# Performance work log

Measured on AMD Instinct MI355X. Metric: run time of the kernel, lower is better.

Reference implementation:

```python
import jax, jax.numpy as jnp
import numpy as np

PI = np.pi
WIN = (8, 8)
N = WIN[0] * WIN[1]          # 64 tokens per window
NUM_HEADS = 8
DIM = 256
HEAD_DIM = DIM // NUM_HEADS  # 32
P = 4                        # Fourier series order (hardcoded in module)
W_RES = 64                   # input_resolution[1]
SCALE = HEAD_DIM ** -0.5
B_ = 1024                    # num_windows * batch


def _azimuth():
    # relative_coords[:, :, 1] from the torch module: relative column offsets
    ch = np.arange(WIN[0])
    cw = np.arange(WIN[1])
    gh, gw = np.meshgrid(ch, cw, indexing='ij')
    cf = np.stack([gh.ravel(), gw.ravel()])          # (2, N)
    rel = cf[:, :, None] - cf[:, None, :]            # (2, N, N)
    return jnp.asarray(rel[1], dtype=jnp.float32)    # (N, N)


def setup_inputs() -> dict:
    key = jax.random.key(0)
    ks = jax.random.split(key, 12)
    std = 0.02
    return {
        'x': jax.random.normal(ks[0], (B_, N, DIM), dtype=jnp.float32),
        'D': jax.random.uniform(ks[1], (B_, N), dtype=jnp.float32),
        'a_p': std * jax.random.normal(ks[2], (P + 1, NUM_HEADS), dtype=jnp.float32),
        'b_p': std * jax.random.normal(ks[3], (P, NUM_HEADS), dtype=jnp.float32),
        'a_r': std * jax.random.normal(ks[4], (P + 1, NUM_HEADS), dtype=jnp.float32),
        'b_r': std * jax.random.normal(ks[5], (P, NUM_HEADS), dtype=jnp.float32),
        'qkv_w': std * jax.random.normal(ks[6], (3 * DIM, DIM), dtype=jnp.float32),
        'qkv_b': jnp.zeros((3 * DIM,), dtype=jnp.float32),
        'proj_w': std * jax.random.normal(ks[7], (DIM, DIM), dtype=jnp.float32),
        'proj_b': jnp.zeros((DIM,), dtype=jnp.float32),
    }


def reference(x, D, a_p, b_p, a_r, b_r, qkv_w, qkv_b, proj_w, proj_b):
    B, n, C = x.shape

    # ---- azimuth Fourier bias: A_phi, shape (H, N, N) ----
    az = _azimuth() * (2.0 * PI / W_RES)                       # (N, N)
    ii = jnp.arange(1, P + 1, dtype=x.dtype)[:, None, None]    # (P, 1, 1)
    cosP = jnp.cos(ii * az)                                    # (P, N, N)
    sinP = jnp.sin(ii * az)
    A_phi = (jnp.einsum('ph,pij->hij', a_p[1:], cosP)
             + jnp.einsum('ph,pij->hij', b_p, sinP)) / P + a_p[0][:, None, None]

    # ---- radius Fourier bias: A_r, shape (B, N, N, H); rad[b,i,j] = D[b,j] - D[b,i] ----
    rad = D[:, None, :] - D[:, :, None]                        # (B, N, N)
    r_max = 2.0                                                # module overwrites r_max = 2
    A_r = jnp.zeros(rad.shape + (NUM_HEADS,), dtype=x.dtype)
    for i in range(1, P + 1):
        arg = rad * (2.0 * PI * i / r_max)
        A_r = A_r + jnp.cos(arg)[..., None] * a_r[i] + jnp.sin(arg)[..., None] * b_r[i - 1]
    A_r = A_r / P + a_r[0]                                     # (B, N, N, H)

    # ---- attention ----
    qkv = (x @ qkv_w.T + qkv_b).reshape(B, n, 3, NUM_HEADS, HEAD_DIM)
    qkv = qkv.transpose(2, 0, 3, 1, 4)                         # (3, B, H, N, hd)
    q, k, v = qkv[0], qkv[1], qkv[2]
    attn = jnp.einsum('bhid,bhjd->bhij', q * SCALE, k)
    attn = attn + A_phi[None] + A_r.transpose(0, 3, 1, 2)
    attn = jax.nn.softmax(attn, axis=-1)
    out = jnp.einsum('bhij,bhjd->bhid', attn, v)
    out = out.transpose(0, 2, 1, 3).reshape(B, n, C)
    return out @ proj_w.T + proj_b
```

## Files before the change

### kernel.cpp

```cpp
#include <hip/hip_runtime.h>
#include <hip/hip_bf16.h>


using short8  = __attribute__((ext_vector_type(8))) short;
using floatx4 = __attribute__((ext_vector_type(4))) float;

#define PI_F    3.14159265358979323846f
#define SCALE_F 0.17677669529663687f

__global__ void prep_kernel(const float* __restrict__ qw,
                            const float* __restrict__ pw,
                            __hip_bfloat16* __restrict__ dst) {
  int g = blockIdx.x * 256 + threadIdx.x;
  const float4* src;
  __hip_bfloat16* d;
  if (g < 49152) { src = (const float4*)qw + g; d = dst + g * 4; }
  else { int g2 = g - 49152; src = (const float4*)pw + g2; d = dst + 196608 + g2 * 4; }
  float4 v = *src;
  d[0] = __float2bfloat16(v.x);
  d[1] = __float2bfloat16(v.y);
  d[2] = __float2bfloat16(v.z);
  d[3] = __float2bfloat16(v.w);
}

__device__ __forceinline__ void fourier_feats(float dv, int col, float* f) {
  float s1, c1; __sincosf(PI_F * dv, &s1, &c1);
  float c2 = c1*c1 - s1*s1, s2 = 2.f*s1*c1;
  float c3 = c2*c1 - s2*s1, s3 = s2*c1 + c2*s1;
  float c4 = c2*c2 - s2*s2, s4 = 2.f*s2*c2;
  float sa1, ca1; __sincosf((2.f * PI_F / 64.f) * (float)col, &sa1, &ca1);
  float ca2 = ca1*ca1 - sa1*sa1, sa2 = 2.f*sa1*ca1;
  float ca3 = ca2*ca1 - sa2*sa1, sa3 = sa2*ca1 + ca2*sa1;
  float ca4 = ca2*ca2 - sa2*sa2, sa4 = 2.f*sa2*ca2;
  f[0]=c1;  f[1]=c2;  f[2]=c3;  f[3]=c4;
  f[4]=s1;  f[5]=s2;  f[6]=s3;  f[7]=s4;
  f[8]=ca1; f[9]=ca2; f[10]=ca3; f[11]=ca4;
  f[12]=sa1; f[13]=sa2; f[14]=sa3; f[15]=sa4;
}

__global__ __launch_bounds__(512, 2) void fused_kernel(
    const float* __restrict__ x, const float* __restrict__ D,
    const float* __restrict__ a_p, const float* __restrict__ b_p,
    const float* __restrict__ a_r, const float* __restrict__ b_r,
    const __hip_bfloat16* __restrict__ wq, const float* __restrict__ qkv_b,
    const __hip_bfloat16* __restrict__ pwb, const float* __restrict__ pb,
    float* __restrict__ out)
{
  constexpr int LDX = 264, LDQ = 264, LDK = 264, LDQf = 40, LDKm = 136,
                LDVt = 72, LDP = 72, LDO = 264;
  __shared__ __align__(16) __hip_bfloat16 sScr[64 * 264];
  __shared__ __align__(16) __hip_bfloat16 sQ  [64 * 264];
  __shared__ __align__(16) __hip_bfloat16 sK  [64 * 264];
  __shared__ __align__(16) __hip_bfloat16 sQf [64 * 40];
  __shared__ __align__(16) __hip_bfloat16 sKm [64 * 136];
  __shared__ __align__(16) __hip_bfloat16 sVt [256 * 72];

  const int tid = threadIdx.x;
  const int lane = tid & 63, w = tid >> 6;
  const int laneN = lane & 15, laneQ = lane >> 4;
  const int b = blockIdx.x;
  const floatx4 fzero = {0.f, 0.f, 0.f, 0.f};
  const short8 zero8 = {0, 0, 0, 0, 0, 0, 0, 0};

  const float4* xg = (const float4*)(x + (size_t)b * 16384);
  #pragma unroll
  for (int it = 0; it < 8; ++it) {
    int g = tid + it * 512;
    float4 v = xg[g];
    int t = g >> 6, c = (g & 63) * 4;
    __hip_bfloat16* p = &sScr[t * LDX + c];
    p[0] = __float2bfloat16(v.x); p[1] = __float2bfloat16(v.y);
    p[2] = __float2bfloat16(v.z); p[3] = __float2bfloat16(v.w);
  }
  if (tid < 64) {
    float f[16];
    fourier_feats(D[b * 64 + tid], tid & 7, f);
    #pragma unroll
    for (int i = 0; i < 16; ++i) sQf[tid * LDQf + i] = __float2bfloat16(f[i]);
    #pragma unroll
    for (int i = 16; i < 32; ++i) sQf[tid * LDQf + i] = __float2bfloat16(0.f);
  }
  __syncthreads();

  {
    int t = tid >> 3, hh = tid & 7;
    float f[16];
    fourier_feats(D[b * 64 + t], t & 7, f);
    #pragma unroll
    for (int p = 0; p < 4; ++p) {
      float ar = a_r[(p + 1) * 8 + hh], br = b_r[p * 8 + hh];
      float ap = a_p[(p + 1) * 8 + hh], bp = b_p[p * 8 + hh];
      float cr = f[p], sr = f[4 + p], ca = f[8 + p], sa = f[12 + p];
      sKm[t * LDKm + hh * 16 +  0 + p] = __float2bfloat16((ar * cr + br * sr) * 0.25f);
      sKm[t * LDKm + hh * 16 +  4 + p] = __float2bfloat16((ar * sr - br * cr) * 0.25f);
      sKm[t * LDKm + hh * 16 +  8 + p] = __float2bfloat16((ap * ca - bp * sa) * 0.25f);
      sKm[t * LDKm + hh * 16 + 12 + p] = __float2bfloat16((ap * sa + bp * ca) * 0.25f);
    }
  }

  short8 afq[4][8];
  #pragma unroll
  for (int mt = 0; mt < 4; ++mt)
    #pragma unroll
    for (int kk = 0; kk < 8; ++kk)
      afq[mt][kk] = *(const short8*)&sScr[(mt * 16 + laneN) * LDX + kk * 32 + laneQ * 8];

  #pragma unroll
  for (int ni = 0; ni < 6; ++ni) {
    int col0 = (w * 6 + ni) * 16;
    float bias = qkv_b[col0 + laneN];
    short8 bq[8];
    #pragma unroll
    for (int kk = 0; kk < 8; ++kk)
      bq[kk] = *(const short8*)&wq[(size_t)(col0 + laneN) * 256 + kk * 32 + laneQ * 8];
    floatx4 acc[4] = {fzero, fzero, fzero, fzero};
    #pragma unroll
    for (int kk = 0; kk < 8; ++kk)
      #pragma unroll
      for (int mt = 0; mt < 4; ++mt)
        acc[mt] = __builtin_amdgcn_mfma_f32_16x16x32_bf16(afq[mt][kk], bq[kk], acc[mt], 0, 0, 0);
    if (col0 < 256) {
      #pragma unroll
      for (int mt = 0; mt < 4; ++mt)
        #pragma unroll
        for (int r = 0; r < 4; ++r)
          sQ[(mt * 16 + laneQ * 4 + r) * LDQ + col0 + laneN] =
              __float2bfloat16((acc[mt][r] + bias) * SCALE_F);
    } else if (col0 < 512) {
      #pragma unroll
      for (int mt = 0; mt < 4; ++mt)
        #pragma unroll
        for (int r = 0; r < 4; ++r)
          sK[(mt * 16 + laneQ * 4 + r) * LDK + (col0 - 256) + laneN] =
              __float2bfloat16(acc[mt][r] + bias);
    } else {
      int vd = col0 - 512 + laneN;
      #pragma unroll
      for (int mt = 0; mt < 4; ++mt)
        #pragma unroll
        for (int r = 0; r < 4; ++r)
          sVt[vd * LDVt + (mt * 16 + laneQ * 4 + r)] = __float2bfloat16(acc[mt][r] + bias);
    }
  }
  __syncthreads();

  const int h = w;
  short8 qf0[4], qf1[4], kf0[4], kf1[4];
  #pragma unroll
  for (int mt = 0; mt < 4; ++mt) {
    qf0[mt] = *(const short8*)&sQ[(mt * 16 + laneN) * LDQ + h * 32 + laneQ * 8];
    qf1[mt] = *(const short8*)&sQf[(mt * 16 + laneN) * LDQf + laneQ * 8];
  }
  #pragma unroll
  for (int nt = 0; nt < 4; ++nt) {
    kf0[nt] = *(const short8*)&sK[(nt * 16 + laneN) * LDK + h * 32 + laneQ * 8];
    short8 km = *(const short8*)&sKm[(nt * 16 + laneN) * LDKm + h * 16 + (laneQ & 1) * 8];
    kf1[nt] = (laneQ < 2) ? km : zero8;
  }
  floatx4 s[4][4];
  #pragma unroll
  for (int mt = 0; mt < 4; ++mt)
    #pragma unroll
    for (int nt = 0; nt < 4; ++nt) {
      s[mt][nt] = __builtin_amdgcn_mfma_f32_16x16x32_bf16(qf0[mt], kf0[nt], fzero, 0, 0, 0);
      s[mt][nt] = __builtin_amdgcn_mfma_f32_16x16x32_bf16(qf1[mt], kf1[nt], s[mt][nt], 0, 0, 0);
    }

  short8 vb[2][2];
  #pragma unroll
  for (int ont = 0; ont < 2; ++ont)
    #pragma unroll
    for (int kk = 0; kk < 2; ++kk)
      vb[ont][kk] = *(const short8*)&sVt[(h * 32 + ont * 16 + laneN) * LDVt + kk * 32 + laneQ * 8];

  floatx4 oacc[4][2];
  __hip_bfloat16* Pw = &sScr[w * 16 * LDP];
  #pragma unroll
  for (int mt = 0; mt < 4; ++mt) {
    #pragma unroll
    for (int r = 0; r < 4; ++r) {
      float mx = fmaxf(fmaxf(s[mt][0][r], s[mt][1][r]), fmaxf(s[mt][2][r], s[mt][3][r]));
      mx = fmaxf(mx, __shfl_xor(mx, 1));
      mx = fmaxf(mx, __shfl_xor(mx, 2));
      mx = fmaxf(mx, __shfl_xor(mx, 4));
      mx = fmaxf(mx, __shfl_xor(mx, 8));
      float e0 = __expf(s[mt][0][r] - mx), e1 = __expf(s[mt][1][r] - mx);
      float e2 = __expf(s[mt][2][r] - mx), e3 = __expf(s[mt][3][r] - mx);
      float sum = e0 + e1 + e2 + e3;
      sum += __shfl_xor(sum, 1);
      sum += __shfl_xor(sum, 2);
      sum += __shfl_xor(sum, 4);
      sum += __shfl_xor(sum, 8);
      float inv = __builtin_amdgcn_rcpf(sum);
      int pr = laneQ * 4 + r;
      Pw[pr * LDP +  0 + laneN] = __float2bfloat16(e0 * inv);
      Pw[pr * LDP + 16 + laneN] = __float2bfloat16(e1 * inv);
      Pw[pr * LDP + 32 + laneN] = __float2bfloat16(e2 * inv);
      Pw[pr * LDP + 48 + laneN] = __float2bfloat16(e3 * inv);
    }
    short8 pf0 = *(const short8*)&Pw[laneN * LDP + laneQ * 8];
    short8 pf1 = *(const short8*)&Pw[laneN * LDP + 32 + laneQ * 8];
    #pragma unroll
    for (int ont = 0; ont < 2; ++ont) {
      oacc[mt][ont] = __builtin_amdgcn_mfma_f32_16x16x32_bf16(pf0, vb[ont][0], fzero, 0, 0, 0);
      oacc[mt][ont] = __builtin_amdgcn_mfma_f32_16x16x32_bf16(pf1, vb[ont][1], oacc[mt][ont], 0, 0, 0);
    }
  }
  __syncthreads();

  #pragma unroll
  for (int mt = 0; mt < 4; ++mt)
    #pragma unroll
    for (int ont = 0; ont < 2; ++ont)
      #pragma unroll
      for (int r = 0; r < 4; ++r)
        sScr[(mt * 16 + laneQ * 4 + r) * LDO + h * 32 + ont * 16 + laneN] =
            __float2bfloat16(oacc[mt][ont][r]);
  __syncthreads();

  const int col0 = w * 32;
  floatx4 pacc[4][2];
  #pragma unroll
  for (int mt = 0; mt < 4; ++mt) { pacc[mt][0] = fzero; pacc[mt][1] = fzero; }
  #pragma unroll
  for (int kk = 0; kk < 8; ++kk) {
    short8 pa[4], pbf[2];
    #pragma unroll
    for (int mt = 0; mt < 4; ++mt)
      pa[mt] = *(const short8*)&sScr[(mt * 16 + laneN) * LDO + kk * 32 + laneQ * 8];
    #pragma unroll
    for (int n2 = 0; n2 < 2; ++n2)
      pbf[n2] = *(const short8*)&pwb[(size_t)(col0 + n2 * 16 + laneN) * 256 + kk * 32 + laneQ * 8];
    #pragma unroll
    for (int mt = 0; mt < 4; ++mt)
      #pragma unroll
      for (int n2 = 0; n2 < 2; ++n2)
        pacc[mt][n2] = __builtin_amdgcn_mfma_f32_16x16x32_bf16(pa[mt], pbf[n2], pacc[mt][n2], 0, 0, 0);
  }
  float bias0 = pb[col0 + laneN], bias1 = pb[col0 + 16 + laneN];
  float* og = out + (size_t)b * 16384;
  #pragma unroll
  for (int mt = 0; mt < 4; ++mt)
    #pragma unroll
    for (int n2 = 0; n2 < 2; ++n2)
      #pragma unroll
      for (int r = 0; r < 4; ++r)
        og[(mt * 16 + laneQ * 4 + r) * 256 + col0 + n2 * 16 + laneN] =
            pacc[mt][n2][r] + (n2 ? bias1 : bias0);
}

extern "C" void kernel_launch(void* const* d_in, const int* in_sizes, int n_in,
                              void* d_out, int out_size, void* d_ws, size_t ws_size,
                              hipStream_t stream) {
  const float* x      = (const float*)d_in[0];
  const float* D      = (const float*)d_in[1];
  const float* a_p    = (const float*)d_in[2];
  const float* b_p    = (const float*)d_in[3];
  const float* a_r    = (const float*)d_in[4];
  const float* b_r    = (const float*)d_in[5];
  const float* qkv_w  = (const float*)d_in[6];
  const float* qkv_b  = (const float*)d_in[7];
  const float* proj_w = (const float*)d_in[8];
  const float* proj_b = (const float*)d_in[9];

  __hip_bfloat16* wq  = (__hip_bfloat16*)d_ws;
  __hip_bfloat16* pwb = wq + 196608;
  float* out = (float*)d_out;

  prep_kernel<<<256, 256, 0, stream>>>(qkv_w, proj_w, wq);
  fused_kernel<<<1024, 512, 0, stream>>>(x, D, a_p, b_p, a_r, b_r, wq, qkv_b,
                                         pwb, proj_b, out);
}
```

Measured before the change: 210.8 us.

## Restructure fused attention to 4 waves, two heads per wave, per-head QKV

Halves the block to 256 threads. Each wave now computes QKV projection columns for its own two heads directly from global x, so the block-wide shared staging of x and the barrier between projection and attention go away. Fourier bias fragments are computed in registers rather than through shared memory, and LDS is shrunk to per-wave Q/K/Vt/P scratch that is reused as the output buffer. The prep kernel packs 8 bf16 per store. In exchange, x is re-read from global/L2 by every wave for each head (eight times per block instead of once), and register pressure rises from the 6x4 accumulators.

```diff
diff --git a/kernel.cpp b/kernel.cpp
--- a/kernel.cpp
+++ b/kernel.cpp
@@ -7,38 +7,30 @@
 
 #define PI_F    3.14159265358979323846f
 #define SCALE_F 0.17677669529663687f
+
+__device__ __forceinline__ short bsh(float x) {
+  __hip_bfloat16 h = __float2bfloat16(x);
+  return *reinterpret_cast<short*>(&h);
+}
+__device__ __forceinline__ short8 pack8(float4 a, float4 b) {
+  short8 r;
+  r[0] = bsh(a.x); r[1] = bsh(a.y); r[2] = bsh(a.z); r[3] = bsh(a.w);
+  r[4] = bsh(b.x); r[5] = bsh(b.y); r[6] = bsh(b.z); r[7] = bsh(b.w);
+  return r;
+}
 
 __global__ void prep_kernel(const float* __restrict__ qw,
                             const float* __restrict__ pw,
                             __hip_bfloat16* __restrict__ dst) {
   int g = blockIdx.x * 256 + threadIdx.x;
   const float4* src;
-  __hip_bfloat16* d;
-  if (g < 49152) { src = (const float4*)qw + g; d = dst + g * 4; }
-  else { int g2 = g - 49152; src = (const float4*)pw + g2; d = dst + 196608 + g2 * 4; }
-  float4 v = *src;
-  d[0] = __float2bfloat16(v.x);
-  d[1] = __float2bfloat16(v.y);
-  d[2] = __float2bfloat16(v.z);
-  d[3] = __float2bfloat16(v.w);
-}
-
-__device__ __forceinline__ void fourier_feats(float dv, int col, float* f) {
-  float s1, c1; __sincosf(PI_F * dv, &s1, &c1);
-  float c2 = c1*c1 - s1*s1, s2 = 2.f*s1*c1;
-  float c3 = c2*c1 - s2*s1, s3 = s2*c1 + c2*s1;
-  float c4 = c2*c2 - s2*s2, s4 = 2.f*s2*c2;
-  float sa1, ca1; __sincosf((2.f * PI_F / 64.f) * (float)col, &sa1, &ca1);
-  float ca2 = ca1*ca1 - sa1*sa1, sa2 = 2.f*sa1*ca1;
-  float ca3 = ca2*ca1 - sa2*sa1, sa3 = sa2*ca1 + ca2*sa1;
-  float ca4 = ca2*ca2 - sa2*sa2, sa4 = 2.f*sa2*ca2;
-  f[0]=c1;  f[1]=c2;  f[2]=c3;  f[3]=c4;
-  f[4]=s1;  f[5]=s2;  f[6]=s3;  f[7]=s4;
-  f[8]=ca1; f[9]=ca2; f[10]=ca3; f[11]=ca4;
-  f[12]=sa1; f[13]=sa2; f[14]=sa3; f[15]=sa4;
-}
-
-__global__ __launch_bounds__(512, 2) void fused_kernel(
+  short8* d;
+  if (g < 24576) { src = (const float4*)qw + 2 * g; d = (short8*)dst + g; }
+  else { int g2 = g - 24576; src = (const float4*)pw + 2 * g2; d = (short8*)(dst + 196608) + g2; }
+  *d = pack8(src[0], src[1]);
+}
+
+__global__ __launch_bounds__(256, 2) void fused_kernel(
     const float* __restrict__ x, const float* __restrict__ D,
     const float* __restrict__ a_p, const float* __restrict__ b_p,
     const float* __restrict__ a_r, const float* __restrict__ b_r,
@@ -46,14 +38,7 @@
     const __hip_bfloat16* __restrict__ pwb, const float* __restrict__ pb,
     float* __restrict__ out)
 {
-  constexpr int LDX = 264, LDQ = 264, LDK = 264, LDQf = 40, LDKm = 136,
-                LDVt = 72, LDP = 72, LDO = 264;
-  __shared__ __align__(16) __hip_bfloat16 sScr[64 * 264];
-  __shared__ __align__(16) __hip_bfloat16 sQ  [64 * 264];
-  __shared__ __align__(16) __hip_bfloat16 sK  [64 * 264];
-  __shared__ __align__(16) __hip_bfloat16 sQf [64 * 40];
-  __shared__ __align__(16) __hip_bfloat16 sKm [64 * 136];
-  __shared__ __align__(16) __hip_bfloat16 sVt [256 * 72];
+  __shared__ __align__(16) __hip_bfloat16 sLds[4 * 7424];
 
   const int tid = threadIdx.x;
   const int lane = tid & 63, w = tid >> 6;
@@ -62,191 +47,222 @@
   const floatx4 fzero = {0.f, 0.f, 0.f, 0.f};
   const short8 zero8 = {0, 0, 0, 0, 0, 0, 0, 0};
 
-  const float4* xg = (const float4*)(x + (size_t)b * 16384);
-  #pragma unroll
-  for (int it = 0; it < 8; ++it) {
-    int g = tid + it * 512;
-    float4 v = xg[g];
-    int t = g >> 6, c = (g & 63) * 4;
-    __hip_bfloat16* p = &sScr[t * LDX + c];
-    p[0] = __float2bfloat16(v.x); p[1] = __float2bfloat16(v.y);
-    p[2] = __float2bfloat16(v.z); p[3] = __float2bfloat16(v.w);
-  }
-  if (tid < 64) {
-    float f[16];
-    fourier_feats(D[b * 64 + tid], tid & 7, f);
-    #pragma unroll
-    for (int i = 0; i < 16; ++i) sQf[tid * LDQf + i] = __float2bfloat16(f[i]);
-    #pragma unroll
-    for (int i = 16; i < 32; ++i) sQf[tid * LDQf + i] = __float2bfloat16(0.f);
-  }
+  __hip_bfloat16* Q  = &sLds[w * 7424];
+  __hip_bfloat16* K  = Q + 2560;
+  __hip_bfloat16* Vt = Q + 5120;
+  __hip_bfloat16* Pp = Q;
+  __hip_bfloat16* sO = &sLds[0];
+
+  const float* xb = x + (size_t)b * 16384;
+
+  float f8[4][8];
+  short8 qf1[4];
+  {
+    float sa1, ca1; __sincosf((2.f * PI_F / 64.f) * (float)(laneN & 7), &sa1, &ca1);
+    float ca2 = ca1*ca1 - sa1*sa1, sa2 = 2.f*sa1*ca1;
+    float ca3 = ca2*ca1 - sa2*sa1, sa3 = sa2*ca1 + ca2*sa1;
+    float ca4 = ca2*ca2 - sa2*sa2, sa4 = 2.f*sa2*ca2;
+    short8 qaz;
+    qaz[0]=bsh(ca1); qaz[1]=bsh(ca2); qaz[2]=bsh(ca3); qaz[3]=bsh(ca4);
+    qaz[4]=bsh(sa1); qaz[5]=bsh(sa2); qaz[6]=bsh(sa3); qaz[7]=bsh(sa4);
+    #pragma unroll
+    for (int tt = 0; tt < 4; ++tt) {
+      float dv = D[b * 64 + tt * 16 + laneN];
+      float s1, c1; __sincosf(PI_F * dv, &s1, &c1);
+      float c2 = c1*c1 - s1*s1, s2 = 2.f*s1*c1;
+      float c3 = c2*c1 - s2*s1, s3 = s2*c1 + c2*s1;
+      float c4 = c2*c2 - s2*s2, s4 = 2.f*s2*c2;
+      if (laneQ == 0) {
+        f8[tt][0]=c1; f8[tt][1]=c2; f8[tt][2]=c3; f8[tt][3]=c4;
+        f8[tt][4]=s1; f8[tt][5]=s2; f8[tt][6]=s3; f8[tt][7]=s4;
+      } else {
+        f8[tt][0]=ca1; f8[tt][1]=ca2; f8[tt][2]=ca3; f8[tt][3]=ca4;
+        f8[tt][4]=sa1; f8[tt][5]=sa2; f8[tt][6]=sa3; f8[tt][7]=sa4;
+      }
+      short8 qrad;
+      qrad[0]=bsh(c1); qrad[1]=bsh(c2); qrad[2]=bsh(c3); qrad[3]=bsh(c4);
+      qrad[4]=bsh(s1); qrad[5]=bsh(s2); qrad[6]=bsh(s3); qrad[7]=bsh(s4);
+      qf1[tt] = (laneQ == 0) ? qrad : ((laneQ == 1) ? qaz : zero8);
+    }
+  }
+
+  floatx4 oacc[2][4][2];
+
+  #pragma unroll
+  for (int hi = 0; hi < 2; ++hi) {
+    const int h = w * 2 + hi;
+
+    int col0s[6];
+    #pragma unroll
+    for (int ni = 0; ni < 6; ++ni)
+      col0s[ni] = (ni < 2) ? h * 32 + ni * 16
+                : (ni < 4) ? 256 + h * 32 + (ni - 2) * 16
+                           : 512 + h * 32 + (ni - 4) * 16;
+    floatx4 acc[6][4];
+    #pragma unroll
+    for (int ni = 0; ni < 6; ++ni)
+      #pragma unroll
+      for (int mt = 0; mt < 4; ++mt) acc[ni][mt] = fzero;
+
+    #pragma unroll
+    for (int kk = 0; kk < 8; ++kk) {
+      short8 a4[4];
+      #pragma unroll
+      for (int mt = 0; mt < 4; ++mt) {
+        const float4* p = (const float4*)(xb + (mt * 16 + laneN) * 256 + kk * 32 + laneQ * 8);
+        a4[mt] = pack8(p[0], p[1]);
+      }
+      #pragma unroll
+      for (int ni = 0; ni < 6; ++ni) {
+        short8 bq = *(const short8*)&wq[(size_t)(col0s[ni] + laneN) * 256 + kk * 32 + laneQ * 8];
+        #pragma unroll
+        for (int mt = 0; mt < 4; ++mt)
+          acc[ni][mt] = __builtin_amdgcn_mfma_f32_16x16x32_bf16(a4[mt], bq, acc[ni][mt], 0, 0, 0);
+      }
+    }
+    #pragma unroll
+    for (int ni = 0; ni < 6; ++ni) {
+      float bias = qkv_b[col0s[ni] + laneN];
+      #pragma unroll
+      for (int mt = 0; mt < 4; ++mt)
+        #pragma unroll
+        for (int r = 0; r < 4; ++r) {
+          int row = mt * 16 + laneQ * 4 + r;
+          float v = acc[ni][mt][r] + bias;
+          if (ni < 2)
+            Q[row * 40 + ni * 16 + laneN] = __float2bfloat16(v * SCALE_F);
+          else if (ni < 4)
+            K[row * 40 + (ni - 2) * 16 + laneN] = __float2bfloat16(v);
+          else
+            Vt[((ni - 4) * 16 + laneN) * 72 + row] = __float2bfloat16(v);
+        }
+    }
+
+    short8 kf1[4];
+    {
+      float A[4], Bp[4];
+      #pragma unroll
+      for (int j = 0; j < 4; ++j) {
+        float arj = a_r[(j + 1) * 8 + h], apj = a_p[(j + 1) * 8 + h];
+        float brj = b_r[j * 8 + h],       bpj = b_p[j * 8 + h];
+        A[j]  = 0.25f * ((laneQ == 0) ? arj : apj);
+        Bp[j] = 0.25f * ((laneQ == 0) ? brj : -bpj);
+      }
+      #pragma unroll
+      for (int tt = 0; tt < 4; ++tt) {
+        short8 m;
+        #pragma unroll
+        for (int j = 0; j < 4; ++j) {
+          m[j]     = bsh(A[j] * f8[tt][j]     + Bp[j] * f8[tt][4 + j]);
+          m[4 + j] = bsh(A[j] * f8[tt][4 + j] - Bp[j] * f8[tt][j]);
+        }
+        kf1[tt] = (laneQ < 2) ? m : zero8;
+      }
+    }
+
+    short8 qf0[4], kf0[4], vb[2][2];
+    #pragma unroll
+    for (int mt = 0; mt < 4; ++mt)
+      qf0[mt] = *(const short8*)&Q[(mt * 16 + laneN) * 40 + laneQ * 8];
+    #pragma unroll
+    for (int nt = 0; nt < 4; ++nt)
+      kf0[nt] = *(const short8*)&K[(nt * 16 + laneN) * 40 + laneQ * 8];
+    #pragma unroll
+    for (int ont = 0; ont < 2; ++ont)
+      #pragma unroll
+      for (int kk = 0; kk < 2; ++kk)
+        vb[ont][kk] = *(const short8*)&Vt[(ont * 16 + laneN) * 72 + kk * 32 + laneQ * 8];
+
+    floatx4 s[4][4];
+    #pragma unroll
+    for (int mt = 0; mt < 4; ++mt)
+      #pragma unroll
+      for (int nt = 0; nt < 4; ++nt) {
+        s[mt][nt] = __builtin_amdgcn_mfma_f32_16x16x32_bf16(qf0[mt], kf0[nt], fzero, 0, 0, 0);
+        s[mt][nt] = __builtin_amdgcn_mfma_f32_16x16x32_bf16(qf1[mt], kf1[nt], s[mt][nt], 0, 0, 0);
+      }
+
+    #pragma unroll
+    for (int mt = 0; mt < 4; ++mt) {
+      #pragma unroll
+      for (int r = 0; r < 4; ++r) {
+        float mx = fmaxf(fmaxf(s[mt][0][r], s[mt][1][r]), fmaxf(s[mt][2][r], s[mt][3][r]));
+        mx = fmaxf(mx, __shfl_xor(mx, 1));
+        mx = fmaxf(mx, __shfl_xor(mx, 2));
+        mx = fmaxf(mx, __shfl_xor(mx, 4));
+        mx = fmaxf(mx, __shfl_xor(mx, 8));
+        float e0 = __expf(s[mt][0][r] - mx), e1 = __expf(s[mt][1][r] - mx);
+        float e2 = __expf(s[mt][2][r] - mx), e3 = __expf(s[mt][3][r] - mx);
+        float sum = e0 + e1 + e2 + e3;
+        sum += __shfl_xor(sum, 1);
+        sum += __shfl_xor(sum, 2);
+        sum += __shfl_xor(sum, 4);
+        sum += __shfl_xor(sum, 8);
+        float inv = __builtin_amdgcn_rcpf(sum);
+        int row = mt * 16 + laneQ * 4 + r;
+        Pp[row * 72 +  0 + laneN] = __float2bfloat16(e0 * inv);
+        Pp[row * 72 + 16 + laneN] = __float2bfloat16(e1 * inv);
+        Pp[row * 72 + 32 + laneN] = __float2bfloat16(e2 * inv);
+        Pp[row * 72 + 48 + laneN] = __float2bfloat16(e3 * inv);
+      }
+    }
+
+    #pragma unroll
+    for (int mt = 0; mt < 4; ++mt) {
+      short8 pf0 = *(const short8*)&Pp[(mt * 16 + laneN) * 72 + laneQ * 8];
+      short8 pf1 = *(const short8*)&Pp[(mt * 16 + laneN) * 72 + 32 + laneQ * 8];
+      #pragma unroll
+      for (int ont = 0; ont < 2; ++ont) {
+        oacc[hi][mt][ont] = __builtin_amdgcn_mfma_f32_16x16x32_bf16(pf0, vb[ont][0], fzero, 0, 0, 0);
+        oacc[hi][mt][ont] = __builtin_amdgcn_mfma_f32_16x16x32_bf16(pf1, vb[ont][1], oacc[hi][mt][ont], 0, 0, 0);
+      }
+    }
+  }
+
   __syncthreads();
-
-  {
-    int t = tid >> 3, hh = tid & 7;
-    float f[16];
-    fourier_feats(D[b * 64 + t], t & 7, f);
-    #pragma unroll
-    for (int p = 0; p < 4; ++p) {
-      float ar = a_r[(p + 1) * 8 + hh], br = b_r[p * 8 + hh];
-      float ap = a_p[(p + 1) * 8 + hh], bp = b_p[p * 8 + hh];
-      float cr = f[p], sr = f[4 + p], ca = f[8 + p], sa = f[12 + p];
-      sKm[t * LDKm + hh * 16 +  0 + p] = __float2bfloat16((ar * cr + br * sr) * 0.25f);
-      sKm[t * LDKm + hh * 16 +  4 + p] = __float2bfloat16((ar * sr - br * cr) * 0.25f);
-      sKm[t * LDKm + hh * 16 +  8 + p] = __float2bfloat16((ap * ca - bp * sa) * 0.25f);
-      sKm[t * LDKm + hh * 16 + 12 + p] = __float2bfloat16((ap * sa + bp * ca) * 0.25f);
-    }
-  }
-
-  short8 afq[4][8];
+  #pragma unroll
+  for (int hi = 0; hi < 2; ++hi)
+    #pragma unroll
+    for (int mt = 0; mt < 4; ++mt)
+      #pragma unroll
+      for (int ont = 0; ont < 2; ++ont)
+        #pragma unroll
+        for (int r = 0; r < 4; ++r)
+          sO[(mt * 16 + laneQ * 4 + r) * 264 + (w * 2 + hi) * 32 + ont * 16 + laneN] =
+              __float2bfloat16(oacc[hi][mt][ont][r]);
+  __syncthreads();
+
+  floatx4 pacc[4][4];
   #pragma unroll
   for (int mt = 0; mt < 4; ++mt)
     #pragma unroll
-    for (int kk = 0; kk < 8; ++kk)
-      afq[mt][kk] = *(const short8*)&sScr[(mt * 16 + laneN) * LDX + kk * 32 + laneQ * 8];
-
-  #pragma unroll
-  for (int ni = 0; ni < 6; ++ni) {
-    int col0 = (w * 6 + ni) * 16;
-    float bias = qkv_b[col0 + laneN];
-    short8 bq[8];
-    #pragma unroll
-    for (int kk = 0; kk < 8; ++kk)
-      bq[kk] = *(const short8*)&wq[(size_t)(col0 + laneN) * 256 + kk * 32 + laneQ * 8];
-    floatx4 acc[4] = {fzero, fzero, fzero, fzero};
-    #pragma unroll
-    for (int kk = 0; kk < 8; ++kk)
-      #pragma unroll
-      for (int mt = 0; mt < 4; ++mt)
-        acc[mt] = __builtin_amdgcn_mfma_f32_16x16x32_bf16(afq[mt][kk], bq[kk], acc[mt], 0, 0, 0);
-    if (col0 < 256) {
-      #pragma unroll
-      for (int mt = 0; mt < 4; ++mt)
-        #pragma unroll
-        for (int r = 0; r < 4; ++r)
-          sQ[(mt * 16 + laneQ * 4 + r) * LDQ + col0 + laneN] =
-              __float2bfloat16((acc[mt][r] + bias) * SCALE_F);
-    } else if (col0 < 512) {
-      #pragma unroll
-      for (int mt = 0; mt < 4; ++mt)
-        #pragma unroll
-        for (int r = 0; r < 4; ++r)
-          sK[(mt * 16 + laneQ * 4 + r) * LDK + (col0 - 256) + laneN] =
-              __float2bfloat16(acc[mt][r] + bias);
-    } else {
-      int vd = col0 - 512 + laneN;
-      #pragma unroll
-      for (int mt = 0; mt < 4; ++mt)
-        #pragma unroll
-        for (int r = 0; r < 4; ++r)
-          sVt[vd * LDVt + (mt * 16 + laneQ * 4 + r)] = __float2bfloat16(acc[mt][r] + bias);
-    }
-  }
-  __syncthreads();
-
-  const int h = w;
-  short8 qf0[4], qf1[4], kf0[4], kf1[4];
-  #pragma unroll
-  for (int mt = 0; mt < 4; ++mt) {
-    qf0[mt] = *(const short8*)&sQ[(mt * 16 + laneN) * LDQ + h * 32 + laneQ * 8];
-    qf1[mt] = *(const short8*)&sQf[(mt * 16 + laneN) * LDQf + laneQ * 8];
-  }
+    for (int nt = 0; nt < 4; ++nt) pacc[mt][nt] = fzero;
+  #pragma unroll
+  for (int kk = 0; kk < 8; ++kk) {
+    short8 pa[4], pbf[4];
+    #pragma unroll
+    for (int mt = 0; mt < 4; ++mt)
+      pa[mt] = *(const short8*)&sO[(mt * 16 + laneN) * 264 + kk * 32 + laneQ * 8];
+    #pragma unroll
+    for (int nt = 0; nt < 4; ++nt)
+      pbf[nt] = *(const short8*)&pwb[(size_t)(w * 64 + nt * 16 + laneN) * 256 + kk * 32 + laneQ * 8];
+    #pragma unroll
+    for (int mt = 0; mt < 4; ++mt)
+      #pragma unroll
+      for (int nt = 0; nt < 4; ++nt)
+        pacc[mt][nt] = __builtin_amdgcn_mfma_f32_16x16x32_bf16(pa[mt], pbf[nt], pacc[mt][nt], 0, 0, 0);
+  }
+  float* og = out + (size_t)b * 16384;
   #pragma unroll
   for (int nt = 0; nt < 4; ++nt) {
-    kf0[nt] = *(const short8*)&sK[(nt * 16 + laneN) * LDK + h * 32 + laneQ * 8];
-    short8 km = *(const short8*)&sKm[(nt * 16 + laneN) * LDKm + h * 16 + (laneQ & 1) * 8];
-    kf1[nt] = (laneQ < 2) ? km : zero8;
-  }
-  floatx4 s[4][4];
-  #pragma unroll
-  for (int mt = 0; mt < 4; ++mt)
-    #pragma unroll
-    for (int nt = 0; nt < 4; ++nt) {
-      s[mt][nt] = __builtin_amdgcn_mfma_f32_16x16x32_bf16(qf0[mt], kf0[nt], fzero, 0, 0, 0);
-      s[mt][nt] = __builtin_amdgcn_mfma_f32_16x16x32_bf16(qf1[mt], kf1[nt], s[mt][nt], 0, 0, 0);
-    }
-
-  short8 vb[2][2];
-  #pragma unroll
-  for (int ont = 0; ont < 2; ++ont)
-    #pragma unroll
-    for (int kk = 0; kk < 2; ++kk)
-      vb[ont][kk] = *(const short8*)&sVt[(h * 32 + ont * 16 + laneN) * LDVt + kk * 32 + laneQ * 8];
-
-  floatx4 oacc[4][2];
-  __hip_bfloat16* Pw = &sScr[w * 16 * LDP];
-  #pragma unroll
-  for (int mt = 0; mt < 4; ++mt) {
-    #pragma unroll
-    for (int r = 0; r < 4; ++r) {
-      float mx = fmaxf(fmaxf(s[mt][0][r], s[mt][1][r]), fmaxf(s[mt][2][r], s[mt][3][r]));
-      mx = fmaxf(mx, __shfl_xor(mx, 1));
-      mx = fmaxf(mx, __shfl_xor(mx, 2));
-      mx = fmaxf(mx, __shfl_xor(mx, 4));
-      mx = fmaxf(mx, __shfl_xor(mx, 8));
-      float e0 = __expf(s[mt][0][r] - mx), e1 = __expf(s[mt][1][r] - mx);
-      float e2 = __expf(s[mt][2][r] - mx), e3 = __expf(s[mt][3][r] - mx);
-      float sum = e0 + e1 + e2 + e3;
-      sum += __shfl_xor(sum, 1);
-      sum += __shfl_xor(sum, 2);
-      sum += __shfl_xor(sum, 4);
-      sum += __shfl_xor(sum, 8);
-      float inv = __builtin_amdgcn_rcpf(sum);
-      int pr = laneQ * 4 + r;
-      Pw[pr * LDP +  0 + laneN] = __float2bfloat16(e0 * inv);
-      Pw[pr * LDP + 16 + laneN] = __float2bfloat16(e1 * inv);
-      Pw[pr * LDP + 32 + laneN] = __float2bfloat16(e2 * inv);
-      Pw[pr * LDP + 48 + laneN] = __float2bfloat16(e3 * inv);
-    }
-    short8 pf0 = *(const short8*)&Pw[laneN * LDP + laneQ * 8];
-    short8 pf1 = *(const short8*)&Pw[laneN * LDP + 32 + laneQ * 8];
-    #pragma unroll
-    for (int ont = 0; ont < 2; ++ont) {
-      oacc[mt][ont] = __builtin_amdgcn_mfma_f32_16x16x32_bf16(pf0, vb[ont][0], fzero, 0, 0, 0);
-      oacc[mt][ont] = __builtin_amdgcn_mfma_f32_16x16x32_bf16(pf1, vb[ont][1], oacc[mt][ont], 0, 0, 0);
-    }
-  }
-  __syncthreads();
-
-  #pragma unroll
-  for (int mt = 0; mt < 4; ++mt)
-    #pragma unroll
-    for (int ont = 0; ont < 2; ++ont)
+    float bias = pb[w * 64 + nt * 16 + laneN];
+    #pragma unroll
+    for (int mt = 0; mt < 4; ++mt)
       #pragma unroll
       for (int r = 0; r < 4; ++r)
-        sScr[(mt * 16 + laneQ * 4 + r) * LDO + h * 32 + ont * 16 + laneN] =
-            __float2bfloat16(oacc[mt][ont][r]);
-  __syncthreads();
-
-  const int col0 = w * 32;
-  floatx4 pacc[4][2];
-  #pragma unroll
-  for (int mt = 0; mt < 4; ++mt) { pacc[mt][0] = fzero; pacc[mt][1] = fzero; }
-  #pragma unroll
-  for (int kk = 0; kk < 8; ++kk) {
-    short8 pa[4], pbf[2];
-    #pragma unroll
-    for (int mt = 0; mt < 4; ++mt)
-      pa[mt] = *(const short8*)&sScr[(mt * 16 + laneN) * LDO + kk * 32 + laneQ * 8];
-    #pragma unroll
-    for (int n2 = 0; n2 < 2; ++n2)
-      pbf[n2] = *(const short8*)&pwb[(size_t)(col0 + n2 * 16 + laneN) * 256 + kk * 32 + laneQ * 8];
-    #pragma unroll
-    for (int mt = 0; mt < 4; ++mt)
-      #pragma unroll
-      for (int n2 = 0; n2 < 2; ++n2)
-        pacc[mt][n2] = __builtin_amdgcn_mfma_f32_16x16x32_bf16(pa[mt], pbf[n2], pacc[mt][n2], 0, 0, 0);
-  }
-  float bias0 = pb[col0 + laneN], bias1 = pb[col0 + 16 + laneN];
-  float* og = out + (size_t)b * 16384;
-  #pragma unroll
-  for (int mt = 0; mt < 4; ++mt)
-    #pragma unroll
-    for (int n2 = 0; n2 < 2; ++n2)
-      #pragma unroll
-      for (int r = 0; r < 4; ++r)
-        og[(mt * 16 + laneQ * 4 + r) * 256 + col0 + n2 * 16 + laneN] =
-            pacc[mt][n2][r] + (n2 ? bias1 : bias0);
+        og[(mt * 16 + laneQ * 4 + r) * 256 + w * 64 + nt * 16 + laneN] =
+            pacc[mt][nt][r] + bias;
+  }
 }
 
 extern "C" void kernel_launch(void* const* d_in, const int* in_sizes, int n_in,
@@ -267,7 +283,7 @@
   __hip_bfloat16* pwb = wq + 196608;
   float* out = (float*)d_out;
 
-  prep_kernel<<<256, 256, 0, stream>>>(qkv_w, proj_w, wq);
-  fused_kernel<<<1024, 512, 0, stream>>>(x, D, a_p, b_p, a_r, b_r, wq, qkv_b,
+  prep_kernel<<<128, 256, 0, stream>>>(qkv_w, proj_w, wq);
+  fused_kernel<<<1024, 256, 0, stream>>>(x, D, a_p, b_p, a_r, b_r, wq, qkv_b,
                                          pwb, proj_b, out);
 }
```

After: 575.4 us. 2.73x slower.
